# Kernel tuning notes

Measured on AMD Instinct MI355X. Metric: run time of the kernel, lower is better.

## Reference

```python
import jax, jax.numpy as jnp
import numpy as np

B, T, DM, D, W, DG = 2, 4096, 2048, 4096, 4, 512  # batch, seq, model hidden, conv channels (value_dim), kernel size, generator hidden


def setup_inputs() -> dict:
    key = jax.random.key(0)
    k0, k1, k2, k3, k4 = jax.random.split(key, 5)
    return {
        "x": jax.random.normal(k0, (B, T, D), jnp.float32) * 0.02,
        "generator_input": jax.random.normal(k1, (B, T, DM), jnp.float32) * 0.02,
        "w1": jax.random.normal(k2, (DG, DM), jnp.float32) * 0.02,   # Linear(DM -> DG), no bias
        "w2": jax.random.normal(k3, (D * W, DG), jnp.float32) * 0.02,  # Linear(DG -> D*W)
        "b2": jax.random.normal(k4, (D * W,), jnp.float32) * 0.02,
    }


def reference(x, generator_input, w1, w2, b2):
    # Hypernetwork: per-token depthwise conv kernels [B, T, D, W]
    h = jax.nn.silu(jnp.einsum("btm,gm->btg", generator_input, w1))
    kflat = jnp.einsum("btg,kg->btk", h, w2) + b2
    kernels = kflat.reshape(x.shape[0], x.shape[1], x.shape[2], W)
    # Causal depthwise conv: left-pad by W-1, windowed multiply-accumulate.
    xp = jnp.pad(x, ((0, 0), (W - 1, 0), (0, 0)))
    Tlen = x.shape[1]
    y = kernels[..., 0] * xp[:, 0:Tlen, :]
    for w in range(1, W):
        y = y + kernels[..., w] * xp[:, w:w + Tlen, :]
    return jax.nn.silu(y)  # [B, T, D]
```

## Files before the change

kernel.cpp:

```cpp
#include <hip/hip_runtime.h>
#include <hip/hip_bf16.h>
#include <stdint.h>

#define TLEN 4096
#define DMm  2048
#define DD   4096
#define DGg  512
#define BT   8192
#define DW   16384

typedef __attribute__((ext_vector_type(8))) short bf16x8;
typedef __attribute__((ext_vector_type(4))) float f32x4;

__device__ __forceinline__ unsigned short f2bf(float f) {
    union { float f; unsigned u; } c; c.f = f;
    unsigned u = c.u;
    unsigned r = (u + 0x7FFFu + ((u >> 16) & 1u)) >> 16;
    return (unsigned short)r;
}

#define NB1 (BT * DMm / 4)
#define NB2 (DGg * DMm / 4)
#define NB3 (DW * DGg / 4)
__global__ void cast_all_kernel(const float* __restrict__ g,
                                const float* __restrict__ w1,
                                const float* __restrict__ w2,
                                unsigned short* __restrict__ o) {
    int i = blockIdx.x * blockDim.x + threadIdx.x;
    if (i >= NB1 + NB2 + NB3) return;
    const float* src; int j = i;
    if (j < NB1) { src = g; }
    else if (j < NB1 + NB2) { src = w1; j -= NB1; }
    else { src = w2; j -= NB1 + NB2; }
    float4 v = reinterpret_cast<const float4*>(src)[j];
    ushort4 u;
    u.x = f2bf(v.x); u.y = f2bf(v.y); u.z = f2bf(v.z); u.w = f2bf(v.w);
    reinterpret_cast<ushort4*>(o)[i] = u;
}

#define GLDS16(gp, lp)                                                         \
    __builtin_amdgcn_global_load_lds(                                          \
        (__attribute__((address_space(1))) const void*)(gp),                   \
        (__attribute__((address_space(3))) void*)(lp), 16, 0, 0)

#define VMCNT(n) asm volatile("s_waitcnt vmcnt(" #n ")" ::: "memory")
#define SBAR()   __builtin_amdgcn_s_barrier()
#define SCHED0() __builtin_amdgcn_sched_barrier(0)

__global__ __launch_bounds__(256) void gemm1_silu_kernel(
    const unsigned short* __restrict__ A,
    const unsigned short* __restrict__ Bm,
    unsigned short* __restrict__ H)
{
    __shared__ short smA[128 * 32];
    __shared__ short smB[128 * 32];
    const int m0   = blockIdx.y * 128;
    const int n0   = blockIdx.x * 128;
    const int lane = threadIdx.x & 63;
    const int wave = threadIdx.x >> 6;
    const int wm   = wave >> 1, wn = wave & 1;

    const int c0 = wave * 64 + lane;
    const int c1 = c0 + 256;
    const int rA0 = m0 + (c0 >> 2), rA1 = m0 + (c1 >> 2);
    const int rB0 = n0 + (c0 >> 2), rB1 = n0 + (c1 >> 2);
    const int ko0 = (c0 & 3) * 8,  ko1 = (c1 & 3) * 8;

    f32x4 acc[4][4] = {};

    for (int k0 = 0; k0 < DMm; k0 += 32) {
        GLDS16(A  + (size_t)rA0 * DMm + k0 + ko0, smA + wave * 512);
        GLDS16(A  + (size_t)rA1 * DMm + k0 + ko1, smA + 2048 + wave * 512);
        GLDS16(Bm + (size_t)rB0 * DMm + k0 + ko0, smB + wave * 512);
        GLDS16(Bm + (size_t)rB1 * DMm + k0 + ko1, smB + 2048 + wave * 512);
        __syncthreads();

        const int la = lane & 15, ko = (lane >> 4) * 8;
        bf16x8 af[4], bfr[4];
#pragma unroll
        for (int mm = 0; mm < 4; ++mm)
            af[mm] = *reinterpret_cast<const bf16x8*>(&smA[(wm * 64 + mm * 16 + la) * 32 + ko]);
#pragma unroll
        for (int nn = 0; nn < 4; ++nn)
            bfr[nn] = *reinterpret_cast<const bf16x8*>(&smB[(wn * 64 + nn * 16 + la) * 32 + ko]);
#pragma unroll
        for (int mm = 0; mm < 4; ++mm)
#pragma unroll
            for (int nn = 0; nn < 4; ++nn)
                acc[mm][nn] = __builtin_amdgcn_mfma_f32_16x16x32_bf16(
                    af[mm], bfr[nn], acc[mm][nn], 0, 0, 0);
        __syncthreads();
    }

#pragma unroll
    for (int mm = 0; mm < 4; ++mm) {
        int rowB = m0 + wm * 64 + mm * 16 + (lane >> 4) * 4;
#pragma unroll
        for (int nn = 0; nn < 4; ++nn) {
            int colG = n0 + wn * 64 + nn * 16 + (lane & 15);
#pragma unroll
            for (int j = 0; j < 4; ++j) {
                float v = acc[mm][nn][j];
                float s = v / (1.0f + __expf(-v));
                H[(size_t)(rowB + j) * DGg + colG] = f2bf(s);
            }
        }
    }
}

#define LDS_B2 65536

__global__ __launch_bounds__(512, 2) void gemm2_conv_silu_kernel(
    const unsigned short* __restrict__ Hb,
    const unsigned short* __restrict__ W2b,
    const float* __restrict__ b2,
    const float* __restrict__ x,
    float* __restrict__ out)
{
    __shared__ __attribute__((aligned(16))) char lds[140080];
    const int tid  = threadIdx.x;
    const int lane = tid & 63, wave = tid >> 6;
    const int wm   = wave >> 2, wn = wave & 3;
    const int la   = lane & 15, hi = lane >> 4;

    int bid = blockIdx.x;
    int swz = (bid & 7) * 256 + (bid >> 3);
    const int n0 = (swz >> 5) * 256;
    const int t0 = (swz & 31) * 256;
    const int d0 = n0 >> 2;

    const int srow = lane >> 2;
    const int scol = ((lane & 3) ^ ((srow >> 1) & 3)) * 8;

    auto stageA = [&](int tk, int p) {
#pragma unroll
        for (int q = 0; q < 2; ++q) {
            int chunk = wave * 2 + q, row = chunk * 16 + srow;
            GLDS16(W2b + (size_t)(n0 + row) * DGg + tk * 32 + scol,
                   lds + p * 16384 + chunk * 1024);
        }
    };
    auto stageB = [&](int tk, int p) {
#pragma unroll
        for (int q = 0; q < 2; ++q) {
            int chunk = wave * 2 + q, row = chunk * 16 + srow;
            GLDS16(Hb + (size_t)(t0 + row) * DGg + tk * 32 + scol,
                   lds + LDS_B2 + p * 16384 + chunk * 1024);
        }
    };

    f32x4 acc[8][4] = {};
    const int slotb = (hi ^ ((la >> 1) & 3)) * 16;
    const int aOff  = (wm * 128 + la) * 64 + slotb;
    const int bOff  = (wn * 64 + la) * 64 + slotb;

    bf16x8 aFa[8], aFb[8];

    auto rdA = [&](bf16x8 (&dst)[8], int p) {
        const char* aB = lds + p * 16384 + aOff;
#pragma unroll
        for (int m = 0; m < 8; ++m)
            dst[m] = *reinterpret_cast<const bf16x8*>(aB + m * 1024);
    };

    auto body = [&](bf16x8 (&AC)[8], bf16x8 (&AN)[8], int pcur, int pnext,
                    int tkS, bool doStage, bool doPre) {
        bf16x8 bF[4];
        const char* bB = lds + LDS_B2 + pcur * 16384 + bOff;
#pragma unroll
        for (int nr = 0; nr < 4; ++nr)
            bF[nr] = *reinterpret_cast<const bf16x8*>(bB + nr * 1024);
        if (doPre) rdA(AN, pnext);
        if (doStage) { stageA(tkS, tkS & 3); stageB(tkS, tkS & 3); }
        SCHED0();
        __builtin_amdgcn_s_setprio(1);
#pragma unroll
        for (int m = 0; m < 8; ++m)
#pragma unroll
            for (int nr = 0; nr < 4; ++nr)
                acc[m][nr] = __builtin_amdgcn_mfma_f32_16x16x32_bf16(
                    AC[m], bF[nr], acc[m][nr], 0, 0, 0);
        __builtin_amdgcn_s_setprio(0);
        SCHED0();
    };

    stageA(0, 0); stageB(0, 0);
    stageA(1, 1); stageB(1, 1);
    stageA(2, 2); stageB(2, 2);
    VMCNT(4);
    SBAR();
    rdA(aFa, 0);

#pragma unroll
    for (int r = 0; r < 13; ++r) {
        if (r & 1) body(aFb, aFa, r & 3, (r + 1) & 3, r + 3, true, true);
        else       body(aFa, aFb, r & 3, (r + 1) & 3, r + 3, true, true);
        VMCNT(4);
        SBAR();
    }
    body(aFb, aFa, 1, 2, 0, false, true);  VMCNT(0); SBAR();
    body(aFa, aFb, 2, 3, 0, false, true);  SBAR();
    body(aFb, aFa, 3, 0, 0, false, false);

    float4 xv[9];
#pragma unroll
    for (int k = 0; k < 9; ++k) {
        int c = tid + k * 512;
        float4 v = make_float4(0.f, 0.f, 0.f, 0.f);
        if (c < 4144) {
            int row = c >> 4, q = c & 15;
            int rg = t0 - 3 + row;
            if (rg >= 0 && (rg >> 12) == (t0 >> 12))
                v = *reinterpret_cast<const float4*>(&x[(size_t)rg * DD + d0 + q * 4]);
        }
        xv[k] = v;
    }
    __syncthreads();

    float* smX = reinterpret_cast<float*>(lds);
#pragma unroll
    for (int k = 0; k < 9; ++k) {
        int c = tid + k * 512;
        if (c < 4144) {
            int row = c >> 4, q = c & 15;
            *reinterpret_cast<float4*>(&smX[row * 68 + q * 4]) = xv[k];
        }
    }
    __syncthreads();

    float4 bb[8];
#pragma unroll
    for (int m = 0; m < 8; ++m)
        bb[m] = *reinterpret_cast<const float4*>(&b2[n0 + wm * 128 + m * 16 + hi * 4]);

    float* smY = reinterpret_cast<float*>(lds + 70448);
#pragma unroll
    for (int nr = 0; nr < 4; ++nr) {
        int tl = wn * 64 + nr * 16 + la;
#pragma unroll
        for (int m = 0; m < 8; ++m) {
            int dl = wm * 32 + m * 4 + hi;
            float pv =
                  (acc[m][nr][0] + bb[m].x) * smX[(tl + 0) * 68 + dl]
                + (acc[m][nr][1] + bb[m].y) * smX[(tl + 1) * 68 + dl]
                + (acc[m][nr][2] + bb[m].z) * smX[(tl + 2) * 68 + dl]
                + (acc[m][nr][3] + bb[m].w) * smX[(tl + 3) * 68 + dl];
            smY[tl * 68 + dl] = pv / (1.0f + __expf(-pv));
        }
    }
    __syncthreads();

    for (int c = tid; c < 256 * 16; c += 512) {
        int row = c >> 4, q = c & 15;
        float4 v = *reinterpret_cast<const float4*>(&smY[row * 68 + q * 4]);
        *reinterpret_cast<float4*>(&out[(size_t)(t0 + row) * DD + d0 + q * 4]) = v;
    }
}

extern "C" void kernel_launch(void* const* d_in, const int* in_sizes, int n_in,
                              void* d_out, int out_size, void* d_ws, size_t ws_size,
                              hipStream_t stream) {
    const float* x   = (const float*)d_in[0];
    const float* gen = (const float*)d_in[1];
    const float* w1  = (const float*)d_in[2];
    const float* w2  = (const float*)d_in[3];
    const float* b2  = (const float*)d_in[4];
    float* out = (float*)d_out;

    char* ws = (char*)d_ws;
    size_t off = 0;
    unsigned short* gen_b = (unsigned short*)(ws + off); off += (size_t)BT * DMm * 2;
    unsigned short* w1_b  = (unsigned short*)(ws + off); off += (size_t)DGg * DMm * 2;
    unsigned short* w2_b  = (unsigned short*)(ws + off); off += (size_t)DW * DGg * 2;
    unsigned short* h_b   = (unsigned short*)(ws + off); off += (size_t)BT * DGg * 2;

    int total4 = NB1 + NB2 + NB3;
    cast_all_kernel<<<(total4 + 255) / 256, 256, 0, stream>>>(gen, w1, w2, gen_b);

    gemm1_silu_kernel<<<dim3(DGg / 128, BT / 128), 256, 0, stream>>>(gen_b, w1_b, h_b);
    gemm2_conv_silu_kernel<<<2048, 512, 0, stream>>>(h_b, w2_b, b2, x, out);
}
```

Before: 261.1 us.

## Restructure GEMM2 main loop into 64-wide K double buffer with split-phase MFMA

Replaces the four-slot 32-wide K ring buffer with two 64-wide K stages, each split into halves. Each half is processed in two phases over the B columns, with global-to-LDS staging spread across the phases. Each phase uses barrier-guarded LDS reads and an explicit lgkmcnt wait before its MFMA burst. The goal is finer interleaving of memory traffic and MFMA work. The cost is roughly double the number of barriers per K step and reloading A fragments with no prefetch overlap.

```diff
diff --git a/kernel.cpp b/kernel.cpp
--- a/kernel.cpp
+++ b/kernel.cpp
@@ -44,6 +44,7 @@
         (__attribute__((address_space(3))) void*)(lp), 16, 0, 0)
 
 #define VMCNT(n) asm volatile("s_waitcnt vmcnt(" #n ")" ::: "memory")
+#define LGKM0()  asm volatile("s_waitcnt lgkmcnt(0)" ::: "memory")
 #define SBAR()   __builtin_amdgcn_s_barrier()
 #define SCHED0() __builtin_amdgcn_sched_barrier(0)
 
@@ -132,75 +133,89 @@
     const int srow = lane >> 2;
     const int scol = ((lane & 3) ^ ((srow >> 1) & 3)) * 8;
 
-    auto stageA = [&](int tk, int p) {
+    auto stageA = [&](int tk, int kh) {
 #pragma unroll
         for (int q = 0; q < 2; ++q) {
             int chunk = wave * 2 + q, row = chunk * 16 + srow;
-            GLDS16(W2b + (size_t)(n0 + row) * DGg + tk * 32 + scol,
-                   lds + p * 16384 + chunk * 1024);
-        }
-    };
-    auto stageB = [&](int tk, int p) {
+            GLDS16(W2b + (size_t)(n0 + row) * DGg + tk * 64 + kh * 32 + scol,
+                   lds + (tk & 1) * 32768 + kh * 16384 + chunk * 1024);
+        }
+    };
+    auto stageB = [&](int tk, int kh) {
 #pragma unroll
         for (int q = 0; q < 2; ++q) {
             int chunk = wave * 2 + q, row = chunk * 16 + srow;
-            GLDS16(Hb + (size_t)(t0 + row) * DGg + tk * 32 + scol,
-                   lds + LDS_B2 + p * 16384 + chunk * 1024);
+            GLDS16(Hb + (size_t)(t0 + row) * DGg + tk * 64 + kh * 32 + scol,
+                   lds + LDS_B2 + (tk & 1) * 32768 + kh * 16384 + chunk * 1024);
         }
     };
 
     f32x4 acc[8][4] = {};
     const int slotb = (hi ^ ((la >> 1) & 3)) * 16;
-    const int aOff  = (wm * 128 + la) * 64 + slotb;
-    const int bOff  = (wn * 64 + la) * 64 + slotb;
-
-    bf16x8 aFa[8], aFb[8];
-
-    auto rdA = [&](bf16x8 (&dst)[8], int p) {
-        const char* aB = lds + p * 16384 + aOff;
+    bf16x8 aF[8];
+
+    auto rdA8 = [&](int par, int kh) {
+        const char* base = lds + par * 32768 + kh * 16384 + (wm * 128 + la) * 64 + slotb;
 #pragma unroll
         for (int m = 0; m < 8; ++m)
-            dst[m] = *reinterpret_cast<const bf16x8*>(aB + m * 1024);
-    };
-
-    auto body = [&](bf16x8 (&AC)[8], bf16x8 (&AN)[8], int pcur, int pnext,
-                    int tkS, bool doStage, bool doPre) {
-        bf16x8 bF[4];
-        const char* bB = lds + LDS_B2 + pcur * 16384 + bOff;
-#pragma unroll
-        for (int nr = 0; nr < 4; ++nr)
-            bF[nr] = *reinterpret_cast<const bf16x8*>(bB + nr * 1024);
-        if (doPre) rdA(AN, pnext);
-        if (doStage) { stageA(tkS, tkS & 3); stageB(tkS, tkS & 3); }
-        SCHED0();
+            aF[m] = *reinterpret_cast<const bf16x8*>(base + m * 1024);
+    };
+
+    auto phase0 = [&](int par, int kh, auto stage, bool v4, bool v0) {
+        rdA8(par, kh);
+        const char* bb = lds + LDS_B2 + par * 32768 + kh * 16384 + (wn * 64 + la) * 64 + slotb;
+        bf16x8 b0 = *reinterpret_cast<const bf16x8*>(bb);
+        bf16x8 b1 = *reinterpret_cast<const bf16x8*>(bb + 1024);
+        stage();
+        if (v4) VMCNT(4);
+        if (v0) VMCNT(0);
+        SBAR(); LGKM0(); SCHED0();
         __builtin_amdgcn_s_setprio(1);
 #pragma unroll
-        for (int m = 0; m < 8; ++m)
-#pragma unroll
-            for (int nr = 0; nr < 4; ++nr)
-                acc[m][nr] = __builtin_amdgcn_mfma_f32_16x16x32_bf16(
-                    AC[m], bF[nr], acc[m][nr], 0, 0, 0);
+        for (int m = 0; m < 8; ++m) {
+            acc[m][0] = __builtin_amdgcn_mfma_f32_16x16x32_bf16(aF[m], b0, acc[m][0], 0, 0, 0);
+            acc[m][1] = __builtin_amdgcn_mfma_f32_16x16x32_bf16(aF[m], b1, acc[m][1], 0, 0, 0);
+        }
         __builtin_amdgcn_s_setprio(0);
-        SCHED0();
-    };
+        SBAR();
+    };
+    auto phase1 = [&](int par, int kh, auto stage, bool v4, bool v0) {
+        const char* bb = lds + LDS_B2 + par * 32768 + kh * 16384 + (wn * 64 + la) * 64 + slotb;
+        bf16x8 b0 = *reinterpret_cast<const bf16x8*>(bb + 2048);
+        bf16x8 b1 = *reinterpret_cast<const bf16x8*>(bb + 3072);
+        stage();
+        if (v4) VMCNT(4);
+        if (v0) VMCNT(0);
+        SBAR(); LGKM0(); SCHED0();
+        __builtin_amdgcn_s_setprio(1);
+#pragma unroll
+        for (int m = 0; m < 8; ++m) {
+            acc[m][2] = __builtin_amdgcn_mfma_f32_16x16x32_bf16(aF[m], b0, acc[m][2], 0, 0, 0);
+            acc[m][3] = __builtin_amdgcn_mfma_f32_16x16x32_bf16(aF[m], b1, acc[m][3], 0, 0, 0);
+        }
+        __builtin_amdgcn_s_setprio(0);
+        SBAR();
+    };
+    auto nostage = [&]() {};
 
     stageA(0, 0); stageB(0, 0);
-    stageA(1, 1); stageB(1, 1);
-    stageA(2, 2); stageB(2, 2);
+    stageA(0, 1); stageB(0, 1);
+    stageA(1, 0); stageB(1, 0);
     VMCNT(4);
     SBAR();
-    rdA(aFa, 0);
-
-#pragma unroll
-    for (int r = 0; r < 13; ++r) {
-        if (r & 1) body(aFb, aFa, r & 3, (r + 1) & 3, r + 3, true, true);
-        else       body(aFa, aFb, r & 3, (r + 1) & 3, r + 3, true, true);
-        VMCNT(4);
-        SBAR();
-    }
-    body(aFb, aFa, 1, 2, 0, false, true);  VMCNT(0); SBAR();
-    body(aFa, aFb, 2, 3, 0, false, true);  SBAR();
-    body(aFb, aFa, 3, 0, 0, false, false);
+
+#pragma unroll
+    for (int i = 0; i < 4; ++i) {
+        const int s2 = 2 * i + 2, s3 = 2 * i + 3;
+        phase0(0, 0, [&]{ stageA(2 * i + 1, 1); }, false, false);
+        phase1(0, 0, [&]{ stageB(2 * i + 1, 1); }, false, false);
+        phase0(0, 1, [&]{ if (s2 < 8) stageA(s2, 0); }, false, false);
+        phase1(0, 1, [&]{ if (s2 < 8) stageB(s2, 0); }, i < 3, i == 3);
+        phase0(1, 0, [&]{ if (s2 < 8) stageA(s2, 1); }, false, false);
+        phase1(1, 0, [&]{ if (s2 < 8) stageB(s2, 1); }, false, false);
+        phase0(1, 1, [&]{ if (s3 < 8) stageA(s3, 0); }, false, false);
+        phase1(1, 1, [&]{ if (s3 < 8) stageB(s3, 0); }, i < 3, false);
+    }
 
     float4 xv[9];
 #pragma unroll
```

Measured after the change: 262.6 us. No clear change (+0.6%).

## Split GEMM2 conv tile across 16 waves with smaller per-wave subtiles

Applied to the files above, without the earlier changes.

The fused GEMM2+conv+SiLU kernel now launches 1024 threads per block instead of 512. Each wave computes a 64x64 accumulator tile instead of 128x64, and each wave stages one 16-row chunk per operand instead of two. The register double-buffered A-fragment prefetch is dropped; A and B fragments are now read from LDS at the start of each k-step. The aim is more resident waves per CU to hide LDS and global latency at lower register pressure, at the cost of more LDS fragment traffic per MFMA and no cross-step A prefetch.

```diff
diff --git a/kernel.cpp b/kernel.cpp
--- a/kernel.cpp
+++ b/kernel.cpp
@@ -110,7 +110,7 @@
 
 #define LDS_B2 65536
 
-__global__ __launch_bounds__(512, 2) void gemm2_conv_silu_kernel(
+__global__ __launch_bounds__(1024, 4) void gemm2_conv_silu_kernel(
     const unsigned short* __restrict__ Hb,
     const unsigned short* __restrict__ W2b,
     const float* __restrict__ b2,
@@ -133,53 +133,41 @@
     const int scol = ((lane & 3) ^ ((srow >> 1) & 3)) * 8;
 
     auto stageA = [&](int tk, int p) {
-#pragma unroll
-        for (int q = 0; q < 2; ++q) {
-            int chunk = wave * 2 + q, row = chunk * 16 + srow;
-            GLDS16(W2b + (size_t)(n0 + row) * DGg + tk * 32 + scol,
-                   lds + p * 16384 + chunk * 1024);
-        }
+        int row = wave * 16 + srow;
+        GLDS16(W2b + (size_t)(n0 + row) * DGg + tk * 32 + scol,
+               lds + p * 16384 + wave * 1024);
     };
     auto stageB = [&](int tk, int p) {
-#pragma unroll
-        for (int q = 0; q < 2; ++q) {
-            int chunk = wave * 2 + q, row = chunk * 16 + srow;
-            GLDS16(Hb + (size_t)(t0 + row) * DGg + tk * 32 + scol,
-                   lds + LDS_B2 + p * 16384 + chunk * 1024);
-        }
+        int row = wave * 16 + srow;
+        GLDS16(Hb + (size_t)(t0 + row) * DGg + tk * 32 + scol,
+               lds + LDS_B2 + p * 16384 + wave * 1024);
     };
 
-    f32x4 acc[8][4] = {};
+    f32x4 acc[4][4] = {};
     const int slotb = (hi ^ ((la >> 1) & 3)) * 16;
-    const int aOff  = (wm * 128 + la) * 64 + slotb;
-    const int bOff  = (wn * 64 + la) * 64 + slotb;
-
-    bf16x8 aFa[8], aFb[8];
-
-    auto rdA = [&](bf16x8 (&dst)[8], int p) {
+    const int aOff  = (wm * 64 + la) * 64 + slotb;
+    const int bOff  = LDS_B2 + (wn * 64 + la) * 64 + slotb;
+
+    auto region = [&](int r, bool doStage) {
+        const int p = r & 3;
         const char* aB = lds + p * 16384 + aOff;
-#pragma unroll
-        for (int m = 0; m < 8; ++m)
-            dst[m] = *reinterpret_cast<const bf16x8*>(aB + m * 1024);
-    };
-
-    auto body = [&](bf16x8 (&AC)[8], bf16x8 (&AN)[8], int pcur, int pnext,
-                    int tkS, bool doStage, bool doPre) {
-        bf16x8 bF[4];
-        const char* bB = lds + LDS_B2 + pcur * 16384 + bOff;
+        const char* bB = lds + p * 16384 + bOff;
+        bf16x8 aF[4], bF[4];
+#pragma unroll
+        for (int m = 0; m < 4; ++m)
+            aF[m] = *reinterpret_cast<const bf16x8*>(aB + m * 1024);
 #pragma unroll
         for (int nr = 0; nr < 4; ++nr)
             bF[nr] = *reinterpret_cast<const bf16x8*>(bB + nr * 1024);
-        if (doPre) rdA(AN, pnext);
-        if (doStage) { stageA(tkS, tkS & 3); stageB(tkS, tkS & 3); }
+        if (doStage) { stageA(r + 3, (r + 3) & 3); stageB(r + 3, (r + 3) & 3); }
         SCHED0();
         __builtin_amdgcn_s_setprio(1);
 #pragma unroll
-        for (int m = 0; m < 8; ++m)
+        for (int m = 0; m < 4; ++m)
 #pragma unroll
             for (int nr = 0; nr < 4; ++nr)
                 acc[m][nr] = __builtin_amdgcn_mfma_f32_16x16x32_bf16(
-                    AC[m], bF[nr], acc[m][nr], 0, 0, 0);
+                    aF[m], bF[nr], acc[m][nr], 0, 0, 0);
         __builtin_amdgcn_s_setprio(0);
         SCHED0();
     };
@@ -189,23 +177,21 @@
     stageA(2, 2); stageB(2, 2);
     VMCNT(4);
     SBAR();
-    rdA(aFa, 0);
 
 #pragma unroll
     for (int r = 0; r < 13; ++r) {
-        if (r & 1) body(aFb, aFa, r & 3, (r + 1) & 3, r + 3, true, true);
-        else       body(aFa, aFb, r & 3, (r + 1) & 3, r + 3, true, true);
+        region(r, true);
         VMCNT(4);
         SBAR();
     }
-    body(aFb, aFa, 1, 2, 0, false, true);  VMCNT(0); SBAR();
-    body(aFa, aFb, 2, 3, 0, false, true);  SBAR();
-    body(aFb, aFa, 3, 0, 0, false, false);
-
-    float4 xv[9];
-#pragma unroll
-    for (int k = 0; k < 9; ++k) {
-        int c = tid + k * 512;
+    region(13, false); VMCNT(2); SBAR();
+    region(14, false); VMCNT(0); SBAR();
+    region(15, false);
+
+    float4 xv[5];
+#pragma unroll
+    for (int k = 0; k < 5; ++k) {
+        int c = tid + k * 1024;
         float4 v = make_float4(0.f, 0.f, 0.f, 0.f);
         if (c < 4144) {
             int row = c >> 4, q = c & 15;
@@ -219,8 +205,8 @@
 
     float* smX = reinterpret_cast<float*>(lds);
 #pragma unroll
-    for (int k = 0; k < 9; ++k) {
-        int c = tid + k * 512;
+    for (int k = 0; k < 5; ++k) {
+        int c = tid + k * 1024;
         if (c < 4144) {
             int row = c >> 4, q = c & 15;
             *reinterpret_cast<float4*>(&smX[row * 68 + q * 4]) = xv[k];
@@ -228,18 +214,18 @@
     }
     __syncthreads();
 
-    float4 bb[8];
-#pragma unroll
-    for (int m = 0; m < 8; ++m)
-        bb[m] = *reinterpret_cast<const float4*>(&b2[n0 + wm * 128 + m * 16 + hi * 4]);
+    float4 bb[4];
+#pragma unroll
+    for (int m = 0; m < 4; ++m)
+        bb[m] = *reinterpret_cast<const float4*>(&b2[n0 + wm * 64 + m * 16 + hi * 4]);
 
     float* smY = reinterpret_cast<float*>(lds + 70448);
 #pragma unroll
     for (int nr = 0; nr < 4; ++nr) {
         int tl = wn * 64 + nr * 16 + la;
 #pragma unroll
-        for (int m = 0; m < 8; ++m) {
-            int dl = wm * 32 + m * 4 + hi;
+        for (int m = 0; m < 4; ++m) {
+            int dl = wm * 16 + m * 4 + hi;
             float pv =
                   (acc[m][nr][0] + bb[m].x) * smX[(tl + 0) * 68 + dl]
                 + (acc[m][nr][1] + bb[m].y) * smX[(tl + 1) * 68 + dl]
@@ -250,7 +236,7 @@
     }
     __syncthreads();
 
-    for (int c = tid; c < 256 * 16; c += 512) {
+    for (int c = tid; c < 256 * 16; c += 1024) {
         int row = c >> 4, q = c & 15;
         float4 v = *reinterpret_cast<const float4*>(&smY[row * 68 + q * 4]);
         *reinterpret_cast<float4*>(&out[(size_t)(t0 + row) * DD + d0 + q * 4]) = v;
@@ -278,5 +264,5 @@
     cast_all_kernel<<<(total4 + 255) / 256, 256, 0, stream>>>(gen, w1, w2, gen_b);
 
     gemm1_silu_kernel<<<dim3(DGg / 128, BT / 128), 256, 0, stream>>>(gen_b, w1_b, h_b);
-    gemm2_conv_silu_kernel<<<2048, 512, 0, stream>>>(h_b, w2_b, b2, x, out);
-}
+    gemm2_conv_silu_kernel<<<2048, 1024, 0, stream>>>(h_b, w2_b, b2, x, out);
+}
```

Result: faster. 253.0 us (-3.1%).
